# Kernel tuning notes

Hardware: AMD Instinct MI355X
Metric: run time of the kernel (lower is better)

## Reference

```python
import jax, jax.numpy as jnp
import numpy as np

N_NODES = 100000


def setup_inputs() -> dict:
    key = jax.random.key(0)
    ks = jax.random.split(key, 9)
    E = 1600000
    x = jax.random.normal(ks[0], (N_NODES, 12), dtype=jnp.float32)
    edge_index = jax.random.randint(ks[1], (2, E), 0, N_NODES, dtype=jnp.int64)
    def glorot(k, shape):
        lim = float(np.sqrt(6.0 / (shape[0] + shape[1])))
        return jax.random.uniform(k, shape, jnp.float32, -lim, lim)
    return {
        "x": x,
        "edge_index": edge_index,
        "W1": glorot(ks[2], (12, 64)),
        "b1": jnp.zeros((64,), jnp.float32),
        "W2": glorot(ks[3], (64, 128)),
        "b2": jnp.zeros((128,), jnp.float32),
        "W3": glorot(ks[4], (128, 96)),
        "b3": jnp.zeros((96,), jnp.float32),
    }


def reference(x, edge_index, W1, b1, W2, b2, W3, b3):
    N = x.shape[0]
    F_channel, n_his = 8, 12
    src, dst = edge_index[0], edge_index[1]
    # add self loops (PyG GCNConv default)
    loop = jnp.arange(N, dtype=src.dtype)
    src = jnp.concatenate([src, loop])
    dst = jnp.concatenate([dst, loop])
    # symmetric normalization: norm_e = deg[src]^-1/2 * deg[dst]^-1/2
    deg = jax.ops.segment_sum(jnp.ones_like(src, dtype=x.dtype), dst, num_segments=N)
    dinv = jnp.where(deg > 0, jax.lax.rsqrt(deg), 0.0)
    norm = dinv[src] * dinv[dst]  # [E+N]

    def gcn(h, W, b):
        hw = h @ W  # transform first (out_ch <= in-edge fanout cost)
        agg = jax.ops.segment_sum(hw[src] * norm[:, None], dst, num_segments=N)
        return agg + b

    h = jax.nn.relu(gcn(x, W1, b1))
    h = jax.nn.relu(gcn(h, W2, b2))
    h = gcn(h, W3, b3)
    return h.reshape(N, F_channel, n_his)
```

## Files before the change

kernel.cpp:

```cpp
#include <hip/hip_runtime.h>
#include <hip/hip_bf16.h>
#include <hip/hip_fp16.h>


static inline int cdiv(int a, int b) { return (a + b - 1) / b; }
constexpr int BLOCK = 256;
constexpr int BSHIFT = 9;
constexpr int BNODES = 1 << BSHIFT;

typedef float nfloat4 __attribute__((ext_vector_type(4)));
typedef _Float16 f16x8 __attribute__((ext_vector_type(8)));
typedef float f32x16 __attribute__((ext_vector_type(16)));


__global__ void zero_int_kernel(int* __restrict__ p, int n) {
    int i = blockIdx.x * blockDim.x + threadIdx.x;
    if (i < n) p[i] = 0;
}

__device__ __forceinline__ void nt_store_raw16(void* p, float4 v) {
    nfloat4 nv;
    nv.x = v.x; nv.y = v.y; nv.z = v.z; nv.w = v.w;
    __builtin_nontemporal_store(nv, (nfloat4*)p);
}

struct h4 { __half2 a, b; };
__device__ __forceinline__ void store_h4(__half* p, float4 v) {
    h4 r;
    r.a = __floats2half2_rn(v.x, v.y);
    r.b = __floats2half2_rn(v.z, v.w);
    *(h4*)p = r;
}

__device__ __forceinline__ void h8_add(float* acc, float4 raw) {
    union { float4 f; __half2 h[4]; } u;
    u.f = raw;
#pragma unroll
    for (int j = 0; j < 4; ++j) {
        float2 p = __half22float2(u.h[j]);
        acc[2 * j] += p.x;
        acc[2 * j + 1] += p.y;
    }
}


template <int CHUNK>
__global__ void bucket_count_kernel(const int* __restrict__ dst, int E,
                                    int* __restrict__ bcnt, int NB) {
    __shared__ int cnt[256];
    for (int i = threadIdx.x; i < NB; i += blockDim.x) cnt[i] = 0;
    __syncthreads();
    const int e0 = blockIdx.x * CHUNK;
    const int e1 = min(e0 + CHUNK, E);
    for (int e = e0 + threadIdx.x; e < e1; e += blockDim.x)
        atomicAdd(&cnt[dst[e] >> BSHIFT], 1);
    __syncthreads();
    for (int i = threadIdx.x; i < NB; i += blockDim.x)
        if (cnt[i]) atomicAdd(&bcnt[i], cnt[i]);
}

__global__ void bucket_scan_kernel(const int* __restrict__ bcnt, int* __restrict__ gbase,
                                   int* __restrict__ gcur, int NB) {
    __shared__ int tmp[256];
    int t = threadIdx.x;
    int v = (t < NB) ? bcnt[t] : 0;
    tmp[t] = v;
    __syncthreads();
    for (int off = 1; off < 256; off <<= 1) {
        int add = (t >= off) ? tmp[t - off] : 0;
        __syncthreads();
        tmp[t] += add;
        __syncthreads();
    }
    if (t < NB) { int ex = tmp[t] - v; gbase[t] = ex; gcur[t] = ex; }
}

template <int CHUNK>
__global__ void bin_edges_kernel(const int* __restrict__ ei, int E,
                                 int* __restrict__ gcur, unsigned* __restrict__ binned,
                                 int NB) {
    __shared__ int cnt[256], base[256], rk[256];
    for (int i = threadIdx.x; i < NB; i += blockDim.x) { cnt[i] = 0; rk[i] = 0; }
    __syncthreads();
    const int e0 = blockIdx.x * CHUNK;
    const int e1 = min(e0 + CHUNK, E);
    for (int e = e0 + threadIdx.x; e < e1; e += blockDim.x)
        atomicAdd(&cnt[ei[E + e] >> BSHIFT], 1);
    __syncthreads();
    for (int i = threadIdx.x; i < NB; i += blockDim.x)
        base[i] = atomicAdd(&gcur[i], cnt[i]);
    __syncthreads();
    for (int e = e0 + threadIdx.x; e < e1; e += blockDim.x) {
        int s = ei[e], d = ei[E + e];
        int b = d >> BSHIFT;
        int r = atomicAdd(&rk[b], 1);
        binned[base[b] + r] = (unsigned)s | ((unsigned)(d & (BNODES - 1)) << 17);
    }
}

__global__ void csr_fill_kernel(const int* __restrict__ gbase, const int* __restrict__ bcnt,
                                const unsigned* __restrict__ binned,
                                int* __restrict__ deg, float* __restrict__ dinv,
                                int* __restrict__ row_ptr, int* __restrict__ csr_src,
                                int* __restrict__ dh, int N) {
    __shared__ int c[BNODES];
    __shared__ int ps[256];
    __shared__ int dhloc[64];
    const int t = threadIdx.x;
    const int b = blockIdx.x;
    const int node0 = b << BSHIFT;
    if (t < BNODES) c[t] = 0;
    if (t < 64) dhloc[t] = 0;
    __syncthreads();
    const int base = gbase[b];
    const int end = base + bcnt[b];
    for (int e = base + t; e < end; e += 1024)
        atomicAdd(&c[binned[e] >> 17], 1);
    __syncthreads();
    int s0 = 0, s1 = 0;
    if (t < 256) {
        s0 = c[2 * t]; s1 = c[2 * t + 1];
        ps[t] = s0 + s1;
    }
    __syncthreads();
    for (int off = 1; off < 256; off <<= 1) {
        int add = (t >= off && t < 256) ? ps[t - off] : 0;
        __syncthreads();
        if (t < 256) ps[t] += add;
        __syncthreads();
    }
    if (t < 256) {
        const int ex = ps[t] - (s0 + s1);
        const int p0 = base + ex;
        const int p1 = p0 + s0;
        const int n0 = node0 + 2 * t;
        if (n0 < N) {
            row_ptr[n0] = p0; deg[n0] = s0; dinv[n0] = rsqrtf((float)s0 + 1.0f);
            atomicAdd(&dhloc[min(s0, 63)], 1);
            if (n0 + 1 < N) {
                row_ptr[n0 + 1] = p1; deg[n0 + 1] = s1; dinv[n0 + 1] = rsqrtf((float)s1 + 1.0f);
                atomicAdd(&dhloc[min(s1, 63)], 1);
            }
        }
        c[2 * t] = p0; c[2 * t + 1] = p1;
    }
    __syncthreads();
    if (t < 64 && dhloc[t]) atomicAdd(&dh[t], dhloc[t]);
    for (int e = base + t; e < end; e += 1024) {
        unsigned sd = binned[e];
        int pos = atomicAdd(&c[sd >> 17], 1);
        csr_src[pos] = (int)(sd & 0x1FFFFu);
    }
}


__global__ void dscan_kernel(int* __restrict__ dh) {
    __shared__ int tmp[64];
    int t = threadIdx.x;
    int v = dh[t];
    tmp[t] = v;
    __syncthreads();
    for (int off = 1; off < 64; off <<= 1) {
        int add = (t >= off) ? tmp[t - off] : 0;
        __syncthreads();
        tmp[t] += add;
        __syncthreads();
    }
    dh[t] = tmp[t] - v;
}

__global__ void dperm_kernel(const int* __restrict__ deg, int* __restrict__ dh,
                             int* __restrict__ perm, int N) {
    __shared__ int cnt[64], base[64], rk[64];
    const int t = threadIdx.x;
    if (t < 64) { cnt[t] = 0; rk[t] = 0; }
    __syncthreads();
    const int i = blockIdx.x * blockDim.x + t;
    const int myb = (i < N) ? min(deg[i], 63) : -1;
    if (myb >= 0) atomicAdd(&cnt[myb], 1);
    __syncthreads();
    if (t < 64) base[t] = cnt[t] ? atomicAdd(&dh[t], cnt[t]) : 0;
    __syncthreads();
    if (myb >= 0) {
        int r = atomicAdd(&rk[myb], 1);
        perm[base[myb] + r] = i;
    }
}

__global__ void hdr_kernel(const int* __restrict__ perm, const int* __restrict__ row_ptr,
                           const int* __restrict__ deg, const float* __restrict__ dinv,
                           int4* __restrict__ hdr, int N) {
    int slot = blockIdx.x * blockDim.x + threadIdx.x;
    if (slot >= N) return;
    int i = perm[N - 1 - slot];
    int4 h;
    h.x = row_ptr[i];
    h.y = deg[i];
    h.z = i;
    h.w = __float_as_int(dinv[i]);
    hdr[slot] = h;
}


__global__ void prescale_h_kernel(const float* __restrict__ x, const float* __restrict__ dinv,
                                  __half* __restrict__ xs, int N) {
    int i = blockIdx.x * blockDim.x + threadIdx.x;
    if (i >= N) return;
    float di = dinv[i];
    const float4* xr = (const float4*)(x + (size_t)i * 12);
    float4 a = xr[0], b = xr[1], c = xr[2];
    union { float4 f; __half2 h[4]; } u0, u1;
    u0.h[0] = __floats2half2_rn(a.x * di, a.y * di);
    u0.h[1] = __floats2half2_rn(a.z * di, a.w * di);
    u0.h[2] = __floats2half2_rn(b.x * di, b.y * di);
    u0.h[3] = __floats2half2_rn(b.z * di, b.w * di);
    u1.h[0] = __floats2half2_rn(c.x * di, c.y * di);
    u1.h[1] = __floats2half2_rn(c.z * di, c.w * di);
    u1.h[2] = __floats2half2_rn(0.f, 0.f);
    u1.h[3] = __floats2half2_rn(0.f, 0.f);
    float4* op = (float4*)(xs + (size_t)i * 16);
    op[0] = u0.f;
    op[1] = u1.f;
}


__device__ __forceinline__ void fma4(float4& acc, float s, const float4& w) {
    acc.x = fmaf(s, w.x, acc.x);
    acc.y = fmaf(s, w.y, acc.y);
    acc.z = fmaf(s, w.z, acc.z);
    acc.w = fmaf(s, w.w, acc.w);
}

__device__ __forceinline__ float4 epilogue4(float4 r, const float* bias, int c0,
                                            bool has_bias, bool relu, bool scale, float di) {
    if (has_bias) {
        const float4 bb = *(const float4*)(bias + c0);
        r.x += bb.x; r.y += bb.y; r.z += bb.z; r.w += bb.w;
    }
    if (relu) {
        r.x = fmaxf(r.x, 0.f); r.y = fmaxf(r.y, 0.f);
        r.z = fmaxf(r.z, 0.f); r.w = fmaxf(r.w, 0.f);
    }
    if (scale) { r.x *= di; r.y *= di; r.z *= di; r.w *= di; }
    return r;
}

template <int IN, int OUT, bool HAS_BIAS, bool RELU, bool SCALE, bool OUT_HALF>
__global__ void transform_kernel(const float* __restrict__ h, const float* __restrict__ W,
                                 const float* __restrict__ bias, const float* __restrict__ dinv,
                                 void* __restrict__ out_v, int N) {
    constexpr int CG = OUT / 4;
    constexpr int THREADS = 8 * CG;
    __shared__ float Ws[IN * OUT];
    for (int i = threadIdx.x; i < IN * OUT / 4; i += THREADS)
        ((float4*)Ws)[i] = ((const float4*)W)[i];
    __syncthreads();

    const int c0 = (threadIdx.x % CG) * 4;
    const int r0 = blockIdx.x * 32 + (threadIdx.x / CG) * 4;
    if (r0 >= N) return;

    const float* __restrict__ hr = h + (size_t)r0 * IN;
    float4 acc[4];
#pragma unroll
    for (int i = 0; i < 4; ++i) acc[i] = make_float4(0.f, 0.f, 0.f, 0.f);

#pragma unroll
    for (int k = 0; k < IN; k += 4) {
        float4 a[4];
#pragma unroll
        for (int i = 0; i < 4; ++i) a[i] = *(const float4*)(hr + (size_t)i * IN + k);
        const float4 w0 = *(const float4*)(Ws + (k + 0) * OUT + c0);
        const float4 w1 = *(const float4*)(Ws + (k + 1) * OUT + c0);
        const float4 w2 = *(const float4*)(Ws + (k + 2) * OUT + c0);
        const float4 w3 = *(const float4*)(Ws + (k + 3) * OUT + c0);
#pragma unroll
        for (int i = 0; i < 4; ++i) {
            fma4(acc[i], a[i].x, w0);
            fma4(acc[i], a[i].y, w1);
            fma4(acc[i], a[i].z, w2);
            fma4(acc[i], a[i].w, w3);
        }
    }

#pragma unroll
    for (int i = 0; i < 4; ++i) {
        float di = SCALE ? dinv[r0 + i] : 0.f;
        float4 r = epilogue4(acc[i], bias, c0, HAS_BIAS, RELU, SCALE, di);
        if (OUT_HALF)
            store_h4((__half*)out_v + (size_t)(r0 + i) * OUT + c0, r);
        else
            *(float4*)((float*)out_v + (size_t)(r0 + i) * OUT + c0) = r;
    }
}


__global__ void prep_w_kernel(const float* __restrict__ W2, const float* __restrict__ W3,
                              __half* __restrict__ W2T, __half* __restrict__ W3T) {
    int i = blockIdx.x * 256 + threadIdx.x;
    if (i < 64 * 128) {
        int k = i >> 7, n = i & 127;
        W2T[n * 64 + k] = __float2half(W2[i]);
    } else {
        int j = i - 64 * 128;
        if (j < 128 * 96) {
            int k = j / 96, n = j - k * 96;
            W3T[n * 128 + k] = __float2half(W3[j]);
        }
    }
}

__global__ void fused_t2t3_kernel(const __half* __restrict__ agg1,
                                  const __half* __restrict__ W2T,
                                  const float* __restrict__ b2,
                                  const __half* __restrict__ W3T,
                                  const float* __restrict__ dinv,
                                  __half* __restrict__ out,
                                  int N) {
    constexpr int LDH = 136;
    __shared__ _Float16 h2s[4][32 * LDH];
    const int lane = threadIdx.x & 63;
    const int wid = threadIdx.x >> 6;
    const int l31 = lane & 31;
    const int lh = lane >> 5;
    _Float16* hs = h2s[wid];

    float b2v[4];
#pragma unroll
    for (int nt = 0; nt < 4; ++nt) b2v[nt] = b2[nt * 32 + l31];

    const int NT = N >> 5;
    for (int t = blockIdx.x * 4 + wid; t < NT; t += gridDim.x * 4) {
        const int r0 = t << 5;

        f16x8 a2[4];
#pragma unroll
        for (int kb = 0; kb < 4; ++kb)
            a2[kb] = *(const f16x8*)(agg1 + (size_t)(r0 + l31) * 64 + kb * 16 + lh * 8);
#pragma unroll
        for (int nt = 0; nt < 4; ++nt) {
            f32x16 c = {0.f, 0.f, 0.f, 0.f, 0.f, 0.f, 0.f, 0.f,
                        0.f, 0.f, 0.f, 0.f, 0.f, 0.f, 0.f, 0.f};
#pragma unroll
            for (int kb = 0; kb < 4; ++kb) {
                f16x8 b = *(const f16x8*)(W2T + (size_t)(nt * 32 + l31) * 64 + kb * 16 + lh * 8);
                c = __builtin_amdgcn_mfma_f32_32x32x16_f16(a2[kb], b, c, 0, 0, 0);
            }
#pragma unroll
            for (int r = 0; r < 16; ++r) {
                int row = (r & 3) + 8 * (r >> 2) + 4 * lh;
                float v = fmaxf(c[r] + b2v[nt], 0.f);
                hs[row * LDH + nt * 32 + l31] = (_Float16)v;
            }
        }

        f16x8 a3[8];
#pragma unroll
        for (int kb = 0; kb < 8; ++kb)
            a3[kb] = *(const f16x8*)(hs + l31 * LDH + kb * 16 + lh * 8);
        float4 dv[4];
#pragma unroll
        for (int rg = 0; rg < 4; ++rg)
            dv[rg] = *(const float4*)(dinv + r0 + rg * 8 + lh * 4);
#pragma unroll
        for (int nt = 0; nt < 3; ++nt) {
            f32x16 c = {0.f, 0.f, 0.f, 0.f, 0.f, 0.f, 0.f, 0.f,
                        0.f, 0.f, 0.f, 0.f, 0.f, 0.f, 0.f, 0.f};
#pragma unroll
            for (int kb = 0; kb < 8; ++kb) {
                f16x8 b = *(const f16x8*)(W3T + (size_t)(nt * 32 + l31) * 128 + kb * 16 + lh * 8);
                c = __builtin_amdgcn_mfma_f32_32x32x16_f16(a3[kb], b, c, 0, 0, 0);
            }
#pragma unroll
            for (int r = 0; r < 16; ++r) {
                int row = (r & 3) + 8 * (r >> 2) + 4 * lh;
                float dvv = ((const float*)&dv[r >> 2])[r & 3];
                hs[row * LDH + nt * 32 + l31] = (_Float16)(c[r] * dvv);
            }
        }

#pragma unroll
        for (int it = 0; it < 6; ++it) {
            int id = lane + it * 64;
            int row = id / 12, ch = id - row * 12;
            float4 v = *(const float4*)(hs + row * LDH + ch * 8);
            *(float4*)((char*)(out + (size_t)r0 * 96) + (size_t)id * 16) = v;
        }
    }
}


__global__ void gather_x_kernel(const int4* __restrict__ hdr, const int* __restrict__ csr_src,
                                const __half* __restrict__ xs,
                                float* __restrict__ out, int N) {
    int t = blockIdx.x * blockDim.x + threadIdx.x;
    if (t >= N * 2) return;
    int slot = t >> 1;
    int c = t & 1;
    const int4 H = hdr[slot];
    const int* __restrict__ sp = csr_src + H.x;
    const int n = H.y;
    const int i = H.z;
    const float di = __int_as_float(H.w);
    int f0 = c * 8;

    float acc[8];
    {
        union { float4 f; __half2 h[4]; } u;
        u.f = *(const float4*)(xs + (size_t)i * 16 + f0);
#pragma unroll
        for (int j = 0; j < 4; ++j) {
            float2 p = __half22float2(u.h[j]);
            acc[2 * j] = p.x; acc[2 * j + 1] = p.y;
        }
    }

    int k = 0;
    if (n >= 8) {
        int s[8];
#pragma unroll
        for (int j = 0; j < 8; ++j) s[j] = sp[j];
        for (; k + 16 <= n; k += 8) {
            int ns[8];
#pragma unroll
            for (int j = 0; j < 8; ++j) ns[j] = sp[k + 8 + j];
            float4 v[8];
#pragma unroll
            for (int j = 0; j < 8; ++j) v[j] = *(const float4*)(xs + (size_t)s[j] * 16 + f0);
#pragma unroll
            for (int j = 0; j < 8; ++j) h8_add(acc, v[j]);
#pragma unroll
            for (int j = 0; j < 8; ++j) s[j] = ns[j];
        }
        float4 v[8];
#pragma unroll
        for (int j = 0; j < 8; ++j) v[j] = *(const float4*)(xs + (size_t)s[j] * 16 + f0);
#pragma unroll
        for (int j = 0; j < 8; ++j) h8_add(acc, v[j]);
        k += 8;
    }
    for (; k + 4 <= n; k += 4) {
        int s0 = sp[k + 0], s1 = sp[k + 1], s2 = sp[k + 2], s3 = sp[k + 3];
        float4 v0 = *(const float4*)(xs + (size_t)s0 * 16 + f0);
        float4 v1 = *(const float4*)(xs + (size_t)s1 * 16 + f0);
        float4 v2 = *(const float4*)(xs + (size_t)s2 * 16 + f0);
        float4 v3 = *(const float4*)(xs + (size_t)s3 * 16 + f0);
        h8_add(acc, v0); h8_add(acc, v1); h8_add(acc, v2); h8_add(acc, v3);
    }
    for (; k < n; ++k) {
        float4 v = *(const float4*)(xs + (size_t)sp[k] * 16 + f0);
        h8_add(acc, v);
    }

    float* op = out + (size_t)i * 12;
    float4 r0;
    r0.x = acc[0] * di; r0.y = acc[1] * di; r0.z = acc[2] * di; r0.w = acc[3] * di;
    if (c == 0) {
        float4 r1;
        r1.x = acc[4] * di; r1.y = acc[5] * di; r1.z = acc[6] * di; r1.w = acc[7] * di;
        *(float4*)op = r0;
        *(float4*)(op + 4) = r1;
    } else {
        *(float4*)(op + 8) = r0;
    }
}

template <int F, bool HAS_BIAS, bool OUT_HALF>
__global__ void gather_h_kernel(const int4* __restrict__ hdr, const int* __restrict__ csr_src,
                                const __half* __restrict__ hws,
                                const float* __restrict__ b, void* __restrict__ out_v, int N) {
    constexpr int TPN = F / 8;
    int t = blockIdx.x * blockDim.x + threadIdx.x;
    if (t >= N * TPN) return;
    int slot = t / TPN;
    int c = t - slot * TPN;
    const int4 H = hdr[slot];
    const int* __restrict__ sp = csr_src + H.x;
    const int n = H.y;
    const int i = H.z;
    const float di = __int_as_float(H.w);
    int f0 = c * 8;

    float acc[8];
    {
        union { float4 f; __half2 h[4]; } u;
        u.f = *(const float4*)(hws + (size_t)i * F + f0);
#pragma unroll
        for (int j = 0; j < 4; ++j) {
            float2 p = __half22float2(u.h[j]);
            acc[2 * j] = p.x; acc[2 * j + 1] = p.y;
        }
    }

    int k = 0;
    if (n >= 8) {
        int s[8];
#pragma unroll
        for (int j = 0; j < 8; ++j) s[j] = sp[j];
        for (; k + 16 <= n; k += 8) {
            int ns[8];
#pragma unroll
            for (int j = 0; j < 8; ++j) ns[j] = sp[k + 8 + j];
            float4 v[8];
#pragma unroll
            for (int j = 0; j < 8; ++j) v[j] = *(const float4*)(hws + (size_t)s[j] * F + f0);
#pragma unroll
            for (int j = 0; j < 8; ++j) h8_add(acc, v[j]);
#pragma unroll
            for (int j = 0; j < 8; ++j) s[j] = ns[j];
        }
        float4 v[8];
#pragma unroll
        for (int j = 0; j < 8; ++j) v[j] = *(const float4*)(hws + (size_t)s[j] * F + f0);
#pragma unroll
        for (int j = 0; j < 8; ++j) h8_add(acc, v[j]);
        k += 8;
    }
    for (; k + 4 <= n; k += 4) {
        int s0 = sp[k + 0], s1 = sp[k + 1], s2 = sp[k + 2], s3 = sp[k + 3];
        float4 v0 = *(const float4*)(hws + (size_t)s0 * F + f0);
        float4 v1 = *(const float4*)(hws + (size_t)s1 * F + f0);
        float4 v2 = *(const float4*)(hws + (size_t)s2 * F + f0);
        float4 v3 = *(const float4*)(hws + (size_t)s3 * F + f0);
        h8_add(acc, v0); h8_add(acc, v1); h8_add(acc, v2); h8_add(acc, v3);
    }
    for (; k < n; ++k) {
        float4 v = *(const float4*)(hws + (size_t)sp[k] * F + f0);
        h8_add(acc, v);
    }

    float4 r0, r1;
    if (HAS_BIAS) {
        const float4 bb0 = *(const float4*)(b + f0);
        const float4 bb1 = *(const float4*)(b + f0 + 4);
        r0.x = fmaf(acc[0], di, bb0.x); r0.y = fmaf(acc[1], di, bb0.y);
        r0.z = fmaf(acc[2], di, bb0.z); r0.w = fmaf(acc[3], di, bb0.w);
        r1.x = fmaf(acc[4], di, bb1.x); r1.y = fmaf(acc[5], di, bb1.y);
        r1.z = fmaf(acc[6], di, bb1.z); r1.w = fmaf(acc[7], di, bb1.w);
    } else {
        r0.x = acc[0] * di; r0.y = acc[1] * di; r0.z = acc[2] * di; r0.w = acc[3] * di;
        r1.x = acc[4] * di; r1.y = acc[5] * di; r1.z = acc[6] * di; r1.w = acc[7] * di;
    }
    if (OUT_HALF) {
        union { float4 f; __half2 h[4]; } u;
        u.h[0] = __floats2half2_rn(r0.x, r0.y);
        u.h[1] = __floats2half2_rn(r0.z, r0.w);
        u.h[2] = __floats2half2_rn(r1.x, r1.y);
        u.h[3] = __floats2half2_rn(r1.z, r1.w);
        nt_store_raw16((__half*)out_v + (size_t)i * F + f0, u.f);
    } else {
        float* op = (float*)out_v + (size_t)i * F + f0;
        nt_store_raw16(op, r0);
        nt_store_raw16(op + 4, r1);
    }
}


extern "C" void kernel_launch(void* const* d_in, const int* in_sizes, int n_in,
                              void* d_out, int out_size, void* d_ws, size_t ws_size,
                              hipStream_t stream) {
    const float* x  = (const float*)d_in[0];
    const int*   ei = (const int*)d_in[1];
    const float* W1 = (const float*)d_in[2];
    const float* b1 = (const float*)d_in[3];
    const float* W2 = (const float*)d_in[4];
    const float* b2 = (const float*)d_in[5];
    const float* W3 = (const float*)d_in[6];
    const float* b3 = (const float*)d_in[7];
    float* out = (float*)d_out;

    const int N = in_sizes[0] / 12;
    const int E = in_sizes[1] / 2;
    const int NB = cdiv(N, BNODES);

    char* ws = (char*)d_ws;
    int*   deg     = (int*)ws;    ws += (size_t)N * sizeof(int);
    int*   row_ptr = (int*)ws;    ws += (size_t)N * sizeof(int);
    int*   perm    = (int*)ws;    ws += (size_t)N * sizeof(int);
    int*   bcnt    = (int*)ws;    ws += 256 * sizeof(int);
    int*   dh      = (int*)ws;    ws += 64 * sizeof(int);
    int*   gbase   = (int*)ws;    ws += 256 * sizeof(int);
    int*   gcur    = (int*)ws;    ws += 256 * sizeof(int);
    float* dinv    = (float*)ws;  ws += (size_t)N * sizeof(float);
    int4*  hdr     = (int4*)ws;   ws += (size_t)N * sizeof(int4);
    __half* W2Th   = (__half*)ws; ws += 128 * 64 * sizeof(__half);
    __half* W3Th   = (__half*)ws; ws += 96 * 128 * sizeof(__half);
    int*   csr_src = (int*)ws;    ws += (size_t)E * sizeof(int);
    float* bufA    = (float*)ws;  ws += (size_t)N * 128 * sizeof(float);
    float* bufB    = (float*)ws;
    unsigned* binned = (unsigned*)bufB;

    zero_int_kernel<<<2, 256, 0, stream>>>(bcnt, 256 + 64);
    prep_w_kernel<<<80, 256, 0, stream>>>(W2, W3, W2Th, W3Th);
    bucket_count_kernel<8192><<<cdiv(E, 8192), BLOCK, 0, stream>>>(ei + E, E, bcnt, NB);
    bucket_scan_kernel<<<1, 256, 0, stream>>>(bcnt, gbase, gcur, NB);
    bin_edges_kernel<8192><<<cdiv(E, 8192), BLOCK, 0, stream>>>(ei, E, gcur, binned, NB);
    csr_fill_kernel<<<NB, 1024, 0, stream>>>(gbase, bcnt, binned, deg, dinv, row_ptr,
                                             csr_src, dh, N);

    dscan_kernel<<<1, 64, 0, stream>>>(dh);
    dperm_kernel<<<cdiv(N, BLOCK), BLOCK, 0, stream>>>(deg, dh, perm, N);
    hdr_kernel<<<cdiv(N, BLOCK), BLOCK, 0, stream>>>(perm, row_ptr, deg, dinv, hdr, N);

    const int tb = cdiv(N, 32);

    prescale_h_kernel<<<cdiv(N, BLOCK), BLOCK, 0, stream>>>(x, dinv, (__half*)bufA, N);
    gather_x_kernel<<<cdiv(N * 2, BLOCK), BLOCK, 0, stream>>>(
        hdr, csr_src, (const __half*)bufA, bufB, N);
    transform_kernel<12, 64, true, true, true, true><<<tb, 8 * (64 / 4), 0, stream>>>(
        bufB, W1, b1, dinv, bufA, N);

    gather_h_kernel<64, false, true><<<cdiv(N * 8, BLOCK), BLOCK, 0, stream>>>(
        hdr, csr_src, (const __half*)bufA, nullptr, bufB, N);

    fused_t2t3_kernel<<<cdiv(N / 32, 8), 256, 0, stream>>>(
        (const __half*)bufB, W2Th, b2, W3Th, dinv, (__half*)bufA, N);

    gather_h_kernel<96, true, false><<<cdiv(N * 12, BLOCK), BLOCK, 0, stream>>>(
        hdr, csr_src, (const __half*)bufA, b3, out, N);
}
```

Measured before the change: 324.0 us.

## Fuse layer-1 gather with W1 transform and merge header build into permutation

Layer-1 neighbour aggregation and the 12->64 transform, with bias, ReLU and dinv scaling, now run in one kernel. Each node's aggregated 12-vector passes through shared memory, so the fp32 intermediate is no longer written and read back. The degree-bucket permutation kernel now writes the node headers directly, which removes the perm array and one launch. The zero kernel becomes a hipMemsetAsync, and the t2t3 grid is doubled, which may change per-block work. The fused kernel adds shared memory and a block barrier inside the gather, and the scattered hdr writes are less coalesced.

```diff
diff --git a/kernel.cpp b/kernel.cpp
--- a/kernel.cpp
+++ b/kernel.cpp
@@ -12,11 +12,6 @@
 typedef _Float16 f16x8 __attribute__((ext_vector_type(8)));
 typedef float f32x16 __attribute__((ext_vector_type(16)));
 
-
-__global__ void zero_int_kernel(int* __restrict__ p, int n) {
-    int i = blockIdx.x * blockDim.x + threadIdx.x;
-    if (i < n) p[i] = 0;
-}
 
 __device__ __forceinline__ void nt_store_raw16(void* p, float4 v) {
     nfloat4 nv;
@@ -169,36 +164,30 @@
     dh[t] = tmp[t] - v;
 }
 
-__global__ void dperm_kernel(const int* __restrict__ deg, int* __restrict__ dh,
-                             int* __restrict__ perm, int N) {
+__global__ void dperm_kernel(const int* __restrict__ deg, const int* __restrict__ row_ptr,
+                             const float* __restrict__ dinv, int* __restrict__ dh,
+                             int4* __restrict__ hdr, int N) {
     __shared__ int cnt[64], base[64], rk[64];
     const int t = threadIdx.x;
     if (t < 64) { cnt[t] = 0; rk[t] = 0; }
     __syncthreads();
     const int i = blockIdx.x * blockDim.x + t;
-    const int myb = (i < N) ? min(deg[i], 63) : -1;
+    const int d = (i < N) ? deg[i] : 0;
+    const int myb = (i < N) ? min(d, 63) : -1;
     if (myb >= 0) atomicAdd(&cnt[myb], 1);
     __syncthreads();
     if (t < 64) base[t] = cnt[t] ? atomicAdd(&dh[t], cnt[t]) : 0;
     __syncthreads();
     if (myb >= 0) {
         int r = atomicAdd(&rk[myb], 1);
-        perm[base[myb] + r] = i;
-    }
-}
-
-__global__ void hdr_kernel(const int* __restrict__ perm, const int* __restrict__ row_ptr,
-                           const int* __restrict__ deg, const float* __restrict__ dinv,
-                           int4* __restrict__ hdr, int N) {
-    int slot = blockIdx.x * blockDim.x + threadIdx.x;
-    if (slot >= N) return;
-    int i = perm[N - 1 - slot];
-    int4 h;
-    h.x = row_ptr[i];
-    h.y = deg[i];
-    h.z = i;
-    h.w = __float_as_int(dinv[i]);
-    hdr[slot] = h;
+        int slot = base[myb] + r;
+        int4 h;
+        h.x = row_ptr[i];
+        h.y = d;
+        h.z = i;
+        h.w = __float_as_int(dinv[i]);
+        hdr[N - 1 - slot] = h;
+    }
 }
 
 
@@ -224,73 +213,110 @@
 }
 
 
-__device__ __forceinline__ void fma4(float4& acc, float s, const float4& w) {
-    acc.x = fmaf(s, w.x, acc.x);
-    acc.y = fmaf(s, w.y, acc.y);
-    acc.z = fmaf(s, w.z, acc.z);
-    acc.w = fmaf(s, w.w, acc.w);
-}
-
-__device__ __forceinline__ float4 epilogue4(float4 r, const float* bias, int c0,
-                                            bool has_bias, bool relu, bool scale, float di) {
-    if (has_bias) {
-        const float4 bb = *(const float4*)(bias + c0);
-        r.x += bb.x; r.y += bb.y; r.z += bb.z; r.w += bb.w;
-    }
-    if (relu) {
-        r.x = fmaxf(r.x, 0.f); r.y = fmaxf(r.y, 0.f);
-        r.z = fmaxf(r.z, 0.f); r.w = fmaxf(r.w, 0.f);
-    }
-    if (scale) { r.x *= di; r.y *= di; r.z *= di; r.w *= di; }
-    return r;
-}
-
-template <int IN, int OUT, bool HAS_BIAS, bool RELU, bool SCALE, bool OUT_HALF>
-__global__ void transform_kernel(const float* __restrict__ h, const float* __restrict__ W,
-                                 const float* __restrict__ bias, const float* __restrict__ dinv,
-                                 void* __restrict__ out_v, int N) {
-    constexpr int CG = OUT / 4;
-    constexpr int THREADS = 8 * CG;
-    __shared__ float Ws[IN * OUT];
-    for (int i = threadIdx.x; i < IN * OUT / 4; i += THREADS)
-        ((float4*)Ws)[i] = ((const float4*)W)[i];
-    __syncthreads();
-
-    const int c0 = (threadIdx.x % CG) * 4;
-    const int r0 = blockIdx.x * 32 + (threadIdx.x / CG) * 4;
-    if (r0 >= N) return;
-
-    const float* __restrict__ hr = h + (size_t)r0 * IN;
-    float4 acc[4];
-#pragma unroll
-    for (int i = 0; i < 4; ++i) acc[i] = make_float4(0.f, 0.f, 0.f, 0.f);
-
-#pragma unroll
-    for (int k = 0; k < IN; k += 4) {
-        float4 a[4];
-#pragma unroll
-        for (int i = 0; i < 4; ++i) a[i] = *(const float4*)(hr + (size_t)i * IN + k);
-        const float4 w0 = *(const float4*)(Ws + (k + 0) * OUT + c0);
-        const float4 w1 = *(const float4*)(Ws + (k + 1) * OUT + c0);
-        const float4 w2 = *(const float4*)(Ws + (k + 2) * OUT + c0);
-        const float4 w3 = *(const float4*)(Ws + (k + 3) * OUT + c0);
-#pragma unroll
-        for (int i = 0; i < 4; ++i) {
-            fma4(acc[i], a[i].x, w0);
-            fma4(acc[i], a[i].y, w1);
-            fma4(acc[i], a[i].z, w2);
-            fma4(acc[i], a[i].w, w3);
-        }
-    }
-
-#pragma unroll
-    for (int i = 0; i < 4; ++i) {
-        float di = SCALE ? dinv[r0 + i] : 0.f;
-        float4 r = epilogue4(acc[i], bias, c0, HAS_BIAS, RELU, SCALE, di);
-        if (OUT_HALF)
-            store_h4((__half*)out_v + (size_t)(r0 + i) * OUT + c0, r);
-        else
-            *(float4*)((float*)out_v + (size_t)(r0 + i) * OUT + c0) = r;
+__global__ void gather_x_t1_kernel(const int4* __restrict__ hdr,
+                                   const int* __restrict__ csr_src,
+                                   const __half* __restrict__ xs,
+                                   const float* __restrict__ W1,
+                                   const float* __restrict__ b1,
+                                   __half* __restrict__ h1h, int N) {
+    __shared__ float W1s[12 * 64];
+    __shared__ float xrow[128][12];
+    const int tid = threadIdx.x;
+    for (int u = tid; u < 12 * 64 / 4; u += 256)
+        ((float4*)W1s)[u] = ((const float4*)W1)[u];
+
+    const int t = blockIdx.x * 256 + tid;
+    const bool valid = (t < N * 2);
+    const int slot = t >> 1;
+    const int c = t & 1;
+    const int nl = tid >> 1;
+    int4 H = valid ? hdr[slot] : make_int4(0, 0, 0, 0);
+    const int* __restrict__ sp = csr_src + H.x;
+    const int n = valid ? H.y : 0;
+    const int i = H.z;
+    const float di = __int_as_float(H.w);
+    const int f0 = c * 8;
+
+    float acc[8];
+    {
+        union { float4 f; __half2 h[4]; } u;
+        u.f = *(const float4*)(xs + (size_t)i * 16 + f0);
+#pragma unroll
+        for (int j = 0; j < 4; ++j) {
+            float2 p = __half22float2(u.h[j]);
+            acc[2 * j] = p.x; acc[2 * j + 1] = p.y;
+        }
+    }
+
+    int k = 0;
+    if (n >= 8) {
+        int s[8];
+#pragma unroll
+        for (int j = 0; j < 8; ++j) s[j] = sp[j];
+        for (; k + 16 <= n; k += 8) {
+            int ns[8];
+#pragma unroll
+            for (int j = 0; j < 8; ++j) ns[j] = sp[k + 8 + j];
+            float4 v[8];
+#pragma unroll
+            for (int j = 0; j < 8; ++j) v[j] = *(const float4*)(xs + (size_t)s[j] * 16 + f0);
+#pragma unroll
+            for (int j = 0; j < 8; ++j) h8_add(acc, v[j]);
+#pragma unroll
+            for (int j = 0; j < 8; ++j) s[j] = ns[j];
+        }
+        float4 v[8];
+#pragma unroll
+        for (int j = 0; j < 8; ++j) v[j] = *(const float4*)(xs + (size_t)s[j] * 16 + f0);
+#pragma unroll
+        for (int j = 0; j < 8; ++j) h8_add(acc, v[j]);
+        k += 8;
+    }
+    for (; k + 4 <= n; k += 4) {
+        int s0 = sp[k + 0], s1 = sp[k + 1], s2 = sp[k + 2], s3 = sp[k + 3];
+        float4 v0 = *(const float4*)(xs + (size_t)s0 * 16 + f0);
+        float4 v1 = *(const float4*)(xs + (size_t)s1 * 16 + f0);
+        float4 v2 = *(const float4*)(xs + (size_t)s2 * 16 + f0);
+        float4 v3 = *(const float4*)(xs + (size_t)s3 * 16 + f0);
+        h8_add(acc, v0); h8_add(acc, v1); h8_add(acc, v2); h8_add(acc, v3);
+    }
+    for (; k < n; ++k) {
+        float4 v = *(const float4*)(xs + (size_t)sp[k] * 16 + f0);
+        h8_add(acc, v);
+    }
+
+    if (valid) {
+        if (c == 0) {
+#pragma unroll
+            for (int j = 0; j < 8; ++j) xrow[nl][j] = acc[j] * di;
+        } else {
+#pragma unroll
+            for (int j = 0; j < 4; ++j) xrow[nl][8 + j] = acc[j] * di;
+        }
+    }
+    __syncthreads();
+    if (!valid) return;
+
+    float xr[12];
+#pragma unroll
+    for (int j = 0; j < 12; ++j) xr[j] = xrow[nl][j];
+
+    __half* op = h1h + (size_t)i * 64 + c * 32;
+#pragma unroll
+    for (int g = 0; g < 8; ++g) {
+        const int c0 = c * 32 + g * 4;
+        float4 r = *(const float4*)(b1 + c0);
+#pragma unroll
+        for (int kk = 0; kk < 12; ++kk) {
+            const float4 w = *(const float4*)(W1s + kk * 64 + c0);
+            r.x = fmaf(xr[kk], w.x, r.x);
+            r.y = fmaf(xr[kk], w.y, r.y);
+            r.z = fmaf(xr[kk], w.z, r.z);
+            r.w = fmaf(xr[kk], w.w, r.w);
+        }
+        r.x = fmaxf(r.x, 0.f) * di; r.y = fmaxf(r.y, 0.f) * di;
+        r.z = fmaxf(r.z, 0.f) * di; r.w = fmaxf(r.w, 0.f) * di;
+        store_h4(op + g * 4, r);
     }
 }
 
@@ -389,81 +415,6 @@
     }
 }
 
-
-__global__ void gather_x_kernel(const int4* __restrict__ hdr, const int* __restrict__ csr_src,
-                                const __half* __restrict__ xs,
-                                float* __restrict__ out, int N) {
-    int t = blockIdx.x * blockDim.x + threadIdx.x;
-    if (t >= N * 2) return;
-    int slot = t >> 1;
-    int c = t & 1;
-    const int4 H = hdr[slot];
-    const int* __restrict__ sp = csr_src + H.x;
-    const int n = H.y;
-    const int i = H.z;
-    const float di = __int_as_float(H.w);
-    int f0 = c * 8;
-
-    float acc[8];
-    {
-        union { float4 f; __half2 h[4]; } u;
-        u.f = *(const float4*)(xs + (size_t)i * 16 + f0);
-#pragma unroll
-        for (int j = 0; j < 4; ++j) {
-            float2 p = __half22float2(u.h[j]);
-            acc[2 * j] = p.x; acc[2 * j + 1] = p.y;
-        }
-    }
-
-    int k = 0;
-    if (n >= 8) {
-        int s[8];
-#pragma unroll
-        for (int j = 0; j < 8; ++j) s[j] = sp[j];
-        for (; k + 16 <= n; k += 8) {
-            int ns[8];
-#pragma unroll
-            for (int j = 0; j < 8; ++j) ns[j] = sp[k + 8 + j];
-            float4 v[8];
-#pragma unroll
-            for (int j = 0; j < 8; ++j) v[j] = *(const float4*)(xs + (size_t)s[j] * 16 + f0);
-#pragma unroll
-            for (int j = 0; j < 8; ++j) h8_add(acc, v[j]);
-#pragma unroll
-            for (int j = 0; j < 8; ++j) s[j] = ns[j];
-        }
-        float4 v[8];
-#pragma unroll
-        for (int j = 0; j < 8; ++j) v[j] = *(const float4*)(xs + (size_t)s[j] * 16 + f0);
-#pragma unroll
-        for (int j = 0; j < 8; ++j) h8_add(acc, v[j]);
-        k += 8;
-    }
-    for (; k + 4 <= n; k += 4) {
-        int s0 = sp[k + 0], s1 = sp[k + 1], s2 = sp[k + 2], s3 = sp[k + 3];
-        float4 v0 = *(const float4*)(xs + (size_t)s0 * 16 + f0);
-        float4 v1 = *(const float4*)(xs + (size_t)s1 * 16 + f0);
-        float4 v2 = *(const float4*)(xs + (size_t)s2 * 16 + f0);
-        float4 v3 = *(const float4*)(xs + (size_t)s3 * 16 + f0);
-        h8_add(acc, v0); h8_add(acc, v1); h8_add(acc, v2); h8_add(acc, v3);
-    }
-    for (; k < n; ++k) {
-        float4 v = *(const float4*)(xs + (size_t)sp[k] * 16 + f0);
-        h8_add(acc, v);
-    }
-
-    float* op = out + (size_t)i * 12;
-    float4 r0;
-    r0.x = acc[0] * di; r0.y = acc[1] * di; r0.z = acc[2] * di; r0.w = acc[3] * di;
-    if (c == 0) {
-        float4 r1;
-        r1.x = acc[4] * di; r1.y = acc[5] * di; r1.z = acc[6] * di; r1.w = acc[7] * di;
-        *(float4*)op = r0;
-        *(float4*)(op + 4) = r1;
-    } else {
-        *(float4*)(op + 8) = r0;
-    }
-}
 
 template <int F, bool HAS_BIAS, bool OUT_HALF>
 __global__ void gather_h_kernel(const int4* __restrict__ hdr, const int* __restrict__ csr_src,
@@ -576,7 +527,6 @@
     char* ws = (char*)d_ws;
     int*   deg     = (int*)ws;    ws += (size_t)N * sizeof(int);
     int*   row_ptr = (int*)ws;    ws += (size_t)N * sizeof(int);
-    int*   perm    = (int*)ws;    ws += (size_t)N * sizeof(int);
     int*   bcnt    = (int*)ws;    ws += 256 * sizeof(int);
     int*   dh      = (int*)ws;    ws += 64 * sizeof(int);
     int*   gbase   = (int*)ws;    ws += 256 * sizeof(int);
@@ -590,7 +540,7 @@
     float* bufB    = (float*)ws;
     unsigned* binned = (unsigned*)bufB;
 
-    zero_int_kernel<<<2, 256, 0, stream>>>(bcnt, 256 + 64);
+    hipMemsetAsync(bcnt, 0, (256 + 64) * sizeof(int), stream);
     prep_w_kernel<<<80, 256, 0, stream>>>(W2, W3, W2Th, W3Th);
     bucket_count_kernel<8192><<<cdiv(E, 8192), BLOCK, 0, stream>>>(ei + E, E, bcnt, NB);
     bucket_scan_kernel<<<1, 256, 0, stream>>>(bcnt, gbase, gcur, NB);
@@ -599,23 +549,18 @@
                                              csr_src, dh, N);
 
     dscan_kernel<<<1, 64, 0, stream>>>(dh);
-    dperm_kernel<<<cdiv(N, BLOCK), BLOCK, 0, stream>>>(deg, dh, perm, N);
-    hdr_kernel<<<cdiv(N, BLOCK), BLOCK, 0, stream>>>(perm, row_ptr, deg, dinv, hdr, N);
-
-    const int tb = cdiv(N, 32);
+    dperm_kernel<<<cdiv(N, BLOCK), BLOCK, 0, stream>>>(deg, row_ptr, dinv, dh, hdr, N);
 
     prescale_h_kernel<<<cdiv(N, BLOCK), BLOCK, 0, stream>>>(x, dinv, (__half*)bufA, N);
-    gather_x_kernel<<<cdiv(N * 2, BLOCK), BLOCK, 0, stream>>>(
-        hdr, csr_src, (const __half*)bufA, bufB, N);
-    transform_kernel<12, 64, true, true, true, true><<<tb, 8 * (64 / 4), 0, stream>>>(
-        bufB, W1, b1, dinv, bufA, N);
+    gather_x_t1_kernel<<<cdiv(N * 2, BLOCK), BLOCK, 0, stream>>>(
+        hdr, csr_src, (const __half*)bufA, W1, b1, (__half*)bufB, N);
 
     gather_h_kernel<64, false, true><<<cdiv(N * 8, BLOCK), BLOCK, 0, stream>>>(
-        hdr, csr_src, (const __half*)bufA, nullptr, bufB, N);
-
-    fused_t2t3_kernel<<<cdiv(N / 32, 8), 256, 0, stream>>>(
-        (const __half*)bufB, W2Th, b2, W3Th, dinv, (__half*)bufA, N);
+        hdr, csr_src, (const __half*)bufB, nullptr, bufA, N);
+
+    fused_t2t3_kernel<<<cdiv(N / 32, 4), 256, 0, stream>>>(
+        (const __half*)bufA, W2Th, b2, W3Th, dinv, (__half*)bufB, N);
 
     gather_h_kernel<96, true, false><<<cdiv(N * 12, BLOCK), BLOCK, 0, stream>>>(
-        hdr, csr_src, (const __half*)bufA, b3, out, N);
-}
+        hdr, csr_src, (const __half*)bufB, b3, out, N);
+}
```

Result: no change. 329.4 us (+1.7%).
